# Kernel optimization log

Hardware: AMD Instinct MI355X
Metric: run time of the kernel (lower is better)

## Reference

```python
import jax, jax.numpy as jnp
import numpy as np

LN_EPS = 1e-5  # torch nn.LayerNorm default


def setup_inputs() -> dict:
    key = jax.random.key(0)
    ks = jax.random.split(key, 8)
    B, S, H, A, L = 32, 2048, 1024, 256, 10
    return {
        "hidden_states": jax.random.normal(ks[0], (B, S, H), dtype=jnp.float32),
        "language_ids": jax.random.randint(ks[1], (B,), 0, L, dtype=jnp.int64),
        "W1": jax.random.normal(ks[2], (L, H, A), dtype=jnp.float32) * (1.0 / np.sqrt(H)),
        "b1": jnp.zeros((L, A), dtype=jnp.float32),
        "W2": jax.random.normal(ks[3], (L, A, H), dtype=jnp.float32) * (1.0 / np.sqrt(A)),
        "b2": jnp.zeros((L, H), dtype=jnp.float32),
        "gamma": jnp.ones((L, H), dtype=jnp.float32),
        "beta": jnp.zeros((L, H), dtype=jnp.float32),
    }


def reference(hidden_states, language_ids, W1, b1, W2, b2, gamma, beta):
    # Gather each sample's language-specific adapter params: [B, ...]
    w1 = W1[language_ids]                       # [B, H, A]
    w2 = W2[language_ids]                       # [B, A, H]
    # Bottleneck MLP (dropout is identity at inference)
    h = jnp.einsum('bsh,bha->bsa', hidden_states, w1) + b1[language_ids][:, None, :]
    h = jax.nn.relu(h)
    adapted = jnp.einsum('bsa,bah->bsh', h, w2) + b2[language_ids][:, None, :]
    # Residual + per-language LayerNorm over last dim
    x = hidden_states + adapted
    mean = jnp.mean(x, axis=-1, keepdims=True)
    var = jnp.mean(jnp.square(x - mean), axis=-1, keepdims=True)
    normed = (x - mean) * jax.lax.rsqrt(var + LN_EPS)
    return normed * gamma[language_ids][:, None, :] + beta[language_ids][:, None, :]
```

## Files before the change

kernel.cpp:

```cpp
#include <hip/hip_runtime.h>

#define B_  32
#define S_  2048
#define H_  1024
#define A_  256
#define L_  10

typedef unsigned short u16;
typedef __bf16 bfv8 __attribute__((ext_vector_type(8)));
typedef float  f32x4 __attribute__((ext_vector_type(4)));

__device__ __forceinline__ u16 f2bf(float f) {
    unsigned int u = __builtin_bit_cast(unsigned int, f);
    u += 0x7FFFu + ((u >> 16) & 1u);
    return (u16)(u >> 16);
}
__device__ __forceinline__ float bf2f(u16 h) {
    unsigned int u = ((unsigned int)h) << 16;
    return __builtin_bit_cast(float, u);
}

__global__ __launch_bounds__(256) void pack_weights(
    const float* __restrict__ W1, const float* __restrict__ W2,
    u16* __restrict__ w1h, u16* __restrict__ w1l,
    u16* __restrict__ w2h, u16* __restrict__ w2l)
{
    int tid = blockIdx.x * 256 + threadIdx.x;
    int which = tid >= L_ * 262144;
    int p = which ? tid - L_ * 262144 : tid;
    int i = p & 7, lane = (p >> 3) & 63, lid = p >> 18;
    int kk = ((lane >> 4) << 3) + i;
    const float* src; u16 *dh, *dl;
    if (!which) {
        int ntkt = (p >> 9) & 511;
        int nt = ntkt & 15, kt = ntkt >> 4;
        int k = kt * 32 + kk, n = nt * 16 + (lane & 15);
        src = W1 + ((size_t)lid * H_ + k) * A_ + n;
        dh = w1h; dl = w1l;
    } else {
        int ntkt = (p >> 9) & 511;
        int nt = ntkt & 63, kt = ntkt >> 6;
        int k = kt * 32 + kk, n = nt * 16 + (lane & 15);
        src = W2 + ((size_t)lid * A_ + k) * H_ + n;
        dh = w2h; dl = w2l;
    }
    float w = *src;
    u16 hi = f2bf(w);
    u16 lo = f2bf(w - bf2f(hi));
    dh[p] = hi; dl[p] = lo;
}

__global__ __launch_bounds__(512) void k_gemm1(
    const float* __restrict__ X, const int* __restrict__ langs,
    const float* __restrict__ b1,
    const u16* __restrict__ w1h, const u16* __restrict__ w1l,
    u16* __restrict__ hh, u16* __restrict__ hl)
{
    __shared__ union {
        struct { u16 xh[64][72]; u16 xl[64][72]; } st;
        float hbuf[64][256];
    } lds;

    const int b   = blockIdx.y;
    const int s0  = blockIdx.x * 64;
    const int lid = langs[b];
    const int t    = threadIdx.x;
    const int lane = t & 63, wid = t >> 6;
    const int wm = wid >> 2, wn = wid & 3;
    const int lr = lane & 15, lg = lane >> 4;

    f32x4 acc[2][4];
    #pragma unroll
    for (int mf = 0; mf < 2; ++mf)
        #pragma unroll
        for (int nf = 0; nf < 4; ++nf) acc[mf][nf] = f32x4{0.f, 0.f, 0.f, 0.f};

    const float* Xb = X + ((size_t)(b * S_ + s0)) * H_;

    #pragma unroll 1
    for (int kc = 0; kc < 16; ++kc) {
        {
            int row = t >> 3, cg = (t & 7) * 8;
            const float* src = Xb + (size_t)row * H_ + kc * 64 + cg;
            float4 v0 = *(const float4*)(src);
            float4 v1 = *(const float4*)(src + 4);
            float vv[8] = {v0.x, v0.y, v0.z, v0.w, v1.x, v1.y, v1.z, v1.w};
            u16* dh = &lds.st.xh[row][cg];
            u16* dl = &lds.st.xl[row][cg];
            #pragma unroll
            for (int j = 0; j < 8; ++j) {
                u16 h = f2bf(vv[j]);
                dh[j] = h; dl[j] = f2bf(vv[j] - bf2f(h));
            }
        }
        __syncthreads();
        #pragma unroll
        for (int kl = 0; kl < 2; ++kl) {
            bfv8 ah[2], al[2];
            #pragma unroll
            for (int mf = 0; mf < 2; ++mf) {
                int row = wm * 32 + mf * 16 + lr;
                int co  = kl * 32 + lg * 8;
                ah[mf] = *(const bfv8*)&lds.st.xh[row][co];
                al[mf] = *(const bfv8*)&lds.st.xl[row][co];
            }
            int ktg = kc * 2 + kl;
            #pragma unroll
            for (int nf = 0; nf < 4; ++nf) {
                int nt = wn * 4 + nf;
                size_t tb = (((size_t)lid * 32 + ktg) * 16 + nt) * 512 + lane * 8;
                bfv8 bh = *(const bfv8*)(w1h + tb);
                bfv8 bl = *(const bfv8*)(w1l + tb);
                #pragma unroll
                for (int mf = 0; mf < 2; ++mf) {
                    acc[mf][nf] = __builtin_amdgcn_mfma_f32_16x16x32_bf16(ah[mf], bh, acc[mf][nf], 0, 0, 0);
                    acc[mf][nf] = __builtin_amdgcn_mfma_f32_16x16x32_bf16(ah[mf], bl, acc[mf][nf], 0, 0, 0);
                    acc[mf][nf] = __builtin_amdgcn_mfma_f32_16x16x32_bf16(al[mf], bh, acc[mf][nf], 0, 0, 0);
                }
            }
        }
        __syncthreads();
    }

    #pragma unroll
    for (int mf = 0; mf < 2; ++mf)
        #pragma unroll
        for (int nf = 0; nf < 4; ++nf) {
            int col = wn * 64 + nf * 16 + lr;
            float bias = b1[lid * A_ + col];
            #pragma unroll
            for (int r = 0; r < 4; ++r) {
                int row = wm * 32 + mf * 16 + lg * 4 + r;
                float v = acc[mf][nf][r] + bias;
                v = v > 0.f ? v : 0.f;
                lds.hbuf[row][col ^ ((row & 7) << 2)] = v;
            }
        }
    __syncthreads();

    size_t base = (((size_t)b * 128 + (s0 >> 4)) * 8) * 512;
    #pragma unroll
    for (int j = 0; j < 32; ++j) {
        int q  = t + j * 512;
        int i  = q & 7, lp = (q >> 3) & 63, kt = (q >> 9) & 7, mt = q >> 12;
        int rowl = mt * 16 + (lp & 15);
        int k    = kt * 32 + ((lp >> 4) << 3) + i;
        float v = lds.hbuf[rowl][k ^ ((rowl & 7) << 2)];
        u16 hi = f2bf(v);
        u16 lo = f2bf(v - bf2f(hi));
        hh[base + q] = hi;
        hl[base + q] = lo;
    }
}

__global__ __launch_bounds__(512) void k_gemm2(
    const float* __restrict__ X, const int* __restrict__ langs,
    const float* __restrict__ b2, const float* __restrict__ gamma,
    const float* __restrict__ beta,
    const u16* __restrict__ w2h, const u16* __restrict__ w2l,
    const u16* __restrict__ hh, const u16* __restrict__ hl,
    float* __restrict__ out)
{
    __shared__ float part[64][4][2];
    __shared__ float mrstd[64][2];

    const int b   = blockIdx.y;
    const int s0  = blockIdx.x * 64;
    const int lid = langs[b];
    const int t    = threadIdx.x;
    const int lane = t & 63, wid = t >> 6;
    const int wm = wid >> 2, wn = wid & 3;
    const int lr = lane & 15, lg = lane >> 4;

    f32x4 acc[2][16];
    #pragma unroll
    for (int mf = 0; mf < 2; ++mf)
        #pragma unroll
        for (int nf = 0; nf < 16; ++nf) acc[mf][nf] = f32x4{0.f, 0.f, 0.f, 0.f};

    size_t habase = (((size_t)b * 128 + (s0 >> 4) + wm * 2) * 8) * 512;

    #pragma unroll 1
    for (int kt = 0; kt < 8; ++kt) {
        bfv8 ah[2], al[2];
        #pragma unroll
        for (int mf = 0; mf < 2; ++mf) {
            size_t tb = habase + ((size_t)mf * 8 + kt) * 512 + lane * 8;
            ah[mf] = *(const bfv8*)(hh + tb);
            al[mf] = *(const bfv8*)(hl + tb);
        }
        #pragma unroll
        for (int nf = 0; nf < 16; ++nf) {
            int nt = wn * 16 + nf;
            size_t tb = (((size_t)lid * 8 + kt) * 64 + nt) * 512 + lane * 8;
            bfv8 bh = *(const bfv8*)(w2h + tb);
            bfv8 bl = *(const bfv8*)(w2l + tb);
            #pragma unroll
            for (int mf = 0; mf < 2; ++mf) {
                acc[mf][nf] = __builtin_amdgcn_mfma_f32_16x16x32_bf16(ah[mf], bh, acc[mf][nf], 0, 0, 0);
                acc[mf][nf] = __builtin_amdgcn_mfma_f32_16x16x32_bf16(ah[mf], bl, acc[mf][nf], 0, 0, 0);
                acc[mf][nf] = __builtin_amdgcn_mfma_f32_16x16x32_bf16(al[mf], bh, acc[mf][nf], 0, 0, 0);
            }
        }
    }

    const float* Xb = X + ((size_t)(b * S_ + s0)) * H_;
    float s1[2][4], s2[2][4];
    #pragma unroll
    for (int mf = 0; mf < 2; ++mf)
        #pragma unroll
        for (int r = 0; r < 4; ++r) { s1[mf][r] = 0.f; s2[mf][r] = 0.f; }

    #pragma unroll
    for (int mf = 0; mf < 2; ++mf)
        #pragma unroll
        for (int nf = 0; nf < 16; ++nf) {
            int col = wn * 256 + nf * 16 + lr;
            float bb = b2[lid * H_ + col];
            #pragma unroll
            for (int r = 0; r < 4; ++r) {
                int row = wm * 32 + mf * 16 + lg * 4 + r;
                float x = acc[mf][nf][r] + bb + Xb[(size_t)row * H_ + col];
                acc[mf][nf][r] = x;
                s1[mf][r] += x; s2[mf][r] += x * x;
            }
        }

    #pragma unroll
    for (int mf = 0; mf < 2; ++mf)
        #pragma unroll
        for (int r = 0; r < 4; ++r) {
            float a = s1[mf][r], c = s2[mf][r];
            #pragma unroll
            for (int m = 1; m < 16; m <<= 1) { a += __shfl_xor(a, m); c += __shfl_xor(c, m); }
            if (lr == 0) {
                int row = wm * 32 + mf * 16 + lg * 4 + r;
                part[row][wn][0] = a; part[row][wn][1] = c;
            }
        }
    __syncthreads();
    if (t < 64) {
        float a = part[t][0][0] + part[t][1][0] + part[t][2][0] + part[t][3][0];
        float c = part[t][0][1] + part[t][1][1] + part[t][2][1] + part[t][3][1];
        float mean = a * (1.f / 1024.f);
        float var  = c * (1.f / 1024.f) - mean * mean;
        mrstd[t][0] = mean;
        mrstd[t][1] = rsqrtf(var + 1e-5f);
    }
    __syncthreads();

    float* ob = out + ((size_t)(b * S_ + s0)) * H_;
    #pragma unroll
    for (int nf = 0; nf < 16; ++nf) {
        int col = wn * 256 + nf * 16 + lr;
        float g  = gamma[lid * H_ + col];
        float bt = beta[lid * H_ + col];
        #pragma unroll
        for (int mf = 0; mf < 2; ++mf)
            #pragma unroll
            for (int r = 0; r < 4; ++r) {
                int row = wm * 32 + mf * 16 + lg * 4 + r;
                float x = acc[mf][nf][r];
                ob[(size_t)row * H_ + col] = (x - mrstd[row][0]) * mrstd[row][1] * g + bt;
            }
    }
}

extern "C" void kernel_launch(void* const* d_in, const int* in_sizes, int n_in,
                              void* d_out, int out_size, void* d_ws, size_t ws_size,
                              hipStream_t stream)
{
    const float* X     = (const float*)d_in[0];
    const int*   langs = (const int*)  d_in[1];
    const float* W1    = (const float*)d_in[2];
    const float* b1    = (const float*)d_in[3];
    const float* W2    = (const float*)d_in[4];
    const float* b2    = (const float*)d_in[5];
    const float* gamma = (const float*)d_in[6];
    const float* beta  = (const float*)d_in[7];
    float* out = (float*)d_out;

    char* ws = (char*)d_ws;
    u16* w1h = (u16*)(ws);
    u16* w1l = (u16*)(ws + 5242880);
    u16* w2h = (u16*)(ws + 10485760);
    u16* w2l = (u16*)(ws + 15728640);
    u16* hh  = (u16*)(ws + 20971520);
    u16* hl  = (u16*)(ws + 54525952);

    hipLaunchKernelGGL(pack_weights, dim3(20480), dim3(256), 0, stream,
                       W1, W2, w1h, w1l, w2h, w2l);
    hipLaunchKernelGGL(k_gemm1, dim3(S_ / 64, B_), dim3(512), 0, stream,
                       X, langs, b1, w1h, w1l, hh, hl);
    hipLaunchKernelGGL(k_gemm2, dim3(S_ / 64, B_), dim3(512), 0, stream,
                       X, langs, b2, gamma, beta, w2h, w2l, hh, hl, out);
}
```

Before: 783.4 us.

## Fuse both adapter GEMMs into one kernel with LDS-staged, double-buffered weights

Merges the two GEMM kernels into one so the bottleneck activation stays in shared memory as split bf16 hi/lo planes instead of going through global memory. Weight tiles are staged into LDS with asynchronous global-to-LDS loads, double-buffered against the MFMA work, and the X tile for the next k-step is prefetched in registers. The packing kernel is rewritten to read weights in coalesced tiles through LDS, and blocks are remapped across batches. In exchange it uses about 148KB of dynamic LDS, which limits occupancy to one block per CU, and adds a barrier per k-step.

```diff
diff --git a/kernel.cpp b/kernel.cpp
--- a/kernel.cpp
+++ b/kernel.cpp
@@ -7,8 +7,10 @@
 #define L_  10
 
 typedef unsigned short u16;
-typedef __bf16 bfv8 __attribute__((ext_vector_type(8)));
+typedef __bf16 bf16_t;
+typedef bf16_t bfv8 __attribute__((ext_vector_type(8)));
 typedef float  f32x4 __attribute__((ext_vector_type(4)));
+typedef u16    u16x4 __attribute__((ext_vector_type(4)));
 
 __device__ __forceinline__ u16 f2bf(float f) {
     unsigned int u = __builtin_bit_cast(unsigned int, f);
@@ -18,6 +20,21 @@
 __device__ __forceinline__ float bf2f(u16 h) {
     unsigned int u = ((unsigned int)h) << 16;
     return __builtin_bit_cast(float, u);
+}
+
+typedef __attribute__((address_space(1))) const unsigned int gu32_t;
+typedef __attribute__((address_space(3))) unsigned int lu32_t;
+__device__ __forceinline__ void glds16(const void* g, void* l) {
+    __builtin_amdgcn_global_load_lds((gu32_t*)g, (lu32_t*)l, 16, 0, 0);
+}
+
+__device__ __forceinline__ void split4(float4 v, u16x4& h4, u16x4& l4) {
+    float a0 = v.x, a1 = v.y, a2 = v.z, a3 = v.w;
+    u16 h;
+    h = f2bf(a0); h4[0] = h; l4[0] = f2bf(a0 - bf2f(h));
+    h = f2bf(a1); h4[1] = h; l4[1] = f2bf(a1 - bf2f(h));
+    h = f2bf(a2); h4[2] = h; l4[2] = f2bf(a2 - bf2f(h));
+    h = f2bf(a3); h4[3] = h; l4[3] = f2bf(a3 - bf2f(h));
 }
 
 __global__ __launch_bounds__(256) void pack_weights(
@@ -25,99 +42,134 @@
     u16* __restrict__ w1h, u16* __restrict__ w1l,
     u16* __restrict__ w2h, u16* __restrict__ w2l)
 {
-    int tid = blockIdx.x * 256 + threadIdx.x;
-    int which = tid >= L_ * 262144;
-    int p = which ? tid - L_ * 262144 : tid;
-    int i = p & 7, lane = (p >> 3) & 63, lid = p >> 18;
-    int kk = ((lane >> 4) << 3) + i;
-    const float* src; u16 *dh, *dl;
-    if (!which) {
-        int ntkt = (p >> 9) & 511;
-        int nt = ntkt & 15, kt = ntkt >> 4;
-        int k = kt * 32 + kk, n = nt * 16 + (lane & 15);
-        src = W1 + ((size_t)lid * H_ + k) * A_ + n;
+    __shared__ float lds[32][264];
+    const int p = blockIdx.x;
+    const float* src; int sstride; u16 *dh, *dl; size_t dbase;
+    if (p < 320) {
+        int lid = p >> 5, ktg = p & 31;
+        src = W1 + ((size_t)lid * H_ + ktg * 32) * A_;
+        sstride = A_;
         dh = w1h; dl = w1l;
+        dbase = (size_t)(lid * 32 + ktg) * 8192;
     } else {
-        int ntkt = (p >> 9) & 511;
-        int nt = ntkt & 63, kt = ntkt >> 6;
-        int k = kt * 32 + kk, n = nt * 16 + (lane & 15);
-        src = W2 + ((size_t)lid * A_ + k) * H_ + n;
+        int p2 = p - 320;
+        int lid = p2 >> 5, kt = (p2 >> 2) & 7, nq = p2 & 3;
+        src = W2 + ((size_t)lid * A_ + kt * 32) * H_ + nq * 256;
+        sstride = H_;
         dh = w2h; dl = w2l;
-    }
-    float w = *src;
-    u16 hi = f2bf(w);
-    u16 lo = f2bf(w - bf2f(hi));
-    dh[p] = hi; dl[p] = lo;
-}
-
-__global__ __launch_bounds__(512) void k_gemm1(
+        dbase = ((size_t)(lid * 8 + kt) * 64 + nq * 16) * 512;
+    }
+    const int t = threadIdx.x;
+    #pragma unroll
+    for (int j = 0; j < 8; ++j) {
+        int row = j * 4 + (t >> 6);
+        int c4  = (t & 63) * 4;
+        float4 v = *(const float4*)(src + (size_t)row * sstride + c4);
+        *(float4*)&lds[row][c4] = v;
+    }
+    __syncthreads();
+    #pragma unroll
+    for (int j = 0; j < 32; ++j) {
+        int q    = j * 256 + t;
+        int slot = q & 511, tl = q >> 9;
+        int ln   = slot >> 3, i = slot & 7;
+        int kl   = ((ln >> 4) << 3) + i;
+        int n    = tl * 16 + (ln & 15);
+        float v  = lds[kl][n];
+        u16 hi   = f2bf(v);
+        dh[dbase + q] = hi;
+        dl[dbase + q] = f2bf(v - bf2f(hi));
+    }
+}
+
+__global__ __launch_bounds__(512) void fused_adapter(
     const float* __restrict__ X, const int* __restrict__ langs,
-    const float* __restrict__ b1,
+    const float* __restrict__ b1, const float* __restrict__ b2,
+    const float* __restrict__ gamma, const float* __restrict__ beta,
     const u16* __restrict__ w1h, const u16* __restrict__ w1l,
-    u16* __restrict__ hh, u16* __restrict__ hl)
+    const u16* __restrict__ w2h, const u16* __restrict__ w2l,
+    float* __restrict__ out)
 {
-    __shared__ union {
-        struct { u16 xh[64][72]; u16 xl[64][72]; } st;
-        float hbuf[64][256];
-    } lds;
-
-    const int b   = blockIdx.y;
-    const int s0  = blockIdx.x * 64;
+    extern __shared__ char smem[];
+    u16*   hh    = (u16*)smem;
+    u16*   hl    = (u16*)(smem + 32768);
+    u16*   xbuf  = (u16*)(smem + 65536);
+    u16*   w1b   = (u16*)(smem + 83968);
+    u16*   w2b   = (u16*)(smem + 65536);
+    float* part  = (float*)(smem + 149504);
+    float* mrstd = (float*)(smem + 151552);
+
+    const int fid = blockIdx.x;
+    const int uu  = fid >> 3;
+    const int b   = (fid & 7) * 4 + (uu >> 5);
+    const int s0  = (uu & 31) * 64;
     const int lid = langs[b];
-    const int t    = threadIdx.x;
-    const int lane = t & 63, wid = t >> 6;
+
+    const int t = threadIdx.x, lane = t & 63, wid = t >> 6;
     const int wm = wid >> 2, wn = wid & 3;
     const int lr = lane & 15, lg = lane >> 4;
 
-    f32x4 acc[2][4];
-    #pragma unroll
-    for (int mf = 0; mf < 2; ++mf)
-        #pragma unroll
-        for (int nf = 0; nf < 4; ++nf) acc[mf][nf] = f32x4{0.f, 0.f, 0.f, 0.f};
-
     const float* Xb = X + ((size_t)(b * S_ + s0)) * H_;
 
+    f32x4 acc1[2][4];
+    #pragma unroll
+    for (int mf = 0; mf < 2; ++mf)
+        #pragma unroll
+        for (int nf = 0; nf < 4; ++nf) acc1[mf][nf] = f32x4{0.f, 0.f, 0.f, 0.f};
+
+    const int srow = t >> 3, skg = (t & 7) * 4;
+
+    {
+        float4 xv = *(const float4*)(Xb + (size_t)srow * H_ + skg);
+        #pragma unroll
+        for (int j = 0; j < 4; ++j) {
+            int idx = wid * 4 + j, pl = idx >> 4, nt = idx & 15;
+            const u16* g = (pl ? w1l : w1h) + ((size_t)(lid * 32 + 0) * 16 + nt) * 512 + lane * 8;
+            glds16(g, w1b + ((0 * 2 + pl) * 16 + nt) * 512);
+        }
+        u16x4 h4, l4; split4(xv, h4, l4);
+        *(u16x4*)(xbuf + srow * 72 + skg)        = h4;
+        *(u16x4*)(xbuf + 4608 + srow * 72 + skg) = l4;
+        __syncthreads();
+    }
+
     #pragma unroll 1
-    for (int kc = 0; kc < 16; ++kc) {
-        {
-            int row = t >> 3, cg = (t & 7) * 8;
-            const float* src = Xb + (size_t)row * H_ + kc * 64 + cg;
-            float4 v0 = *(const float4*)(src);
-            float4 v1 = *(const float4*)(src + 4);
-            float vv[8] = {v0.x, v0.y, v0.z, v0.w, v1.x, v1.y, v1.z, v1.w};
-            u16* dh = &lds.st.xh[row][cg];
-            u16* dl = &lds.st.xl[row][cg];
-            #pragma unroll
-            for (int j = 0; j < 8; ++j) {
-                u16 h = f2bf(vv[j]);
-                dh[j] = h; dl[j] = f2bf(vv[j] - bf2f(h));
+    for (int kt = 0; kt < 32; ++kt) {
+        float4 xv;
+        if (kt < 31) {
+            xv = *(const float4*)(Xb + (size_t)srow * H_ + (kt + 1) * 32 + skg);
+            #pragma unroll
+            for (int j = 0; j < 4; ++j) {
+                int idx = wid * 4 + j, pl = idx >> 4, nt = idx & 15;
+                const u16* g = (pl ? w1l : w1h) + ((size_t)(lid * 32 + kt + 1) * 16 + nt) * 512 + lane * 8;
+                glds16(g, w1b + ((((kt + 1) & 1) * 2 + pl) * 16 + nt) * 512);
+            }
+        }
+        bfv8 ah[2], al[2];
+        #pragma unroll
+        for (int mf = 0; mf < 2; ++mf) {
+            int row = wm * 32 + mf * 16 + lr;
+            ah[mf] = *(const bfv8*)(xbuf + row * 72 + lg * 8);
+            al[mf] = *(const bfv8*)(xbuf + 4608 + row * 72 + lg * 8);
+        }
+        const u16* wb = w1b + (kt & 1) * 16384;
+        #pragma unroll
+        for (int nf = 0; nf < 4; ++nf) {
+            int nt = wn * 4 + nf;
+            bfv8 bh = *(const bfv8*)(wb + nt * 512 + lane * 8);
+            bfv8 bl = *(const bfv8*)(wb + 8192 + nt * 512 + lane * 8);
+            #pragma unroll
+            for (int mf = 0; mf < 2; ++mf) {
+                acc1[mf][nf] = __builtin_amdgcn_mfma_f32_16x16x32_bf16(ah[mf], bh, acc1[mf][nf], 0, 0, 0);
+                acc1[mf][nf] = __builtin_amdgcn_mfma_f32_16x16x32_bf16(ah[mf], bl, acc1[mf][nf], 0, 0, 0);
+                acc1[mf][nf] = __builtin_amdgcn_mfma_f32_16x16x32_bf16(al[mf], bh, acc1[mf][nf], 0, 0, 0);
             }
         }
         __syncthreads();
-        #pragma unroll
-        for (int kl = 0; kl < 2; ++kl) {
-            bfv8 ah[2], al[2];
-            #pragma unroll
-            for (int mf = 0; mf < 2; ++mf) {
-                int row = wm * 32 + mf * 16 + lr;
-                int co  = kl * 32 + lg * 8;
-                ah[mf] = *(const bfv8*)&lds.st.xh[row][co];
-                al[mf] = *(const bfv8*)&lds.st.xl[row][co];
-            }
-            int ktg = kc * 2 + kl;
-            #pragma unroll
-            for (int nf = 0; nf < 4; ++nf) {
-                int nt = wn * 4 + nf;
-                size_t tb = (((size_t)lid * 32 + ktg) * 16 + nt) * 512 + lane * 8;
-                bfv8 bh = *(const bfv8*)(w1h + tb);
-                bfv8 bl = *(const bfv8*)(w1l + tb);
-                #pragma unroll
-                for (int mf = 0; mf < 2; ++mf) {
-                    acc[mf][nf] = __builtin_amdgcn_mfma_f32_16x16x32_bf16(ah[mf], bh, acc[mf][nf], 0, 0, 0);
-                    acc[mf][nf] = __builtin_amdgcn_mfma_f32_16x16x32_bf16(ah[mf], bl, acc[mf][nf], 0, 0, 0);
-                    acc[mf][nf] = __builtin_amdgcn_mfma_f32_16x16x32_bf16(al[mf], bh, acc[mf][nf], 0, 0, 0);
-                }
-            }
+        if (kt < 31) {
+            u16x4 h4, l4; split4(xv, h4, l4);
+            *(u16x4*)(xbuf + srow * 72 + skg)        = h4;
+            *(u16x4*)(xbuf + 4608 + srow * 72 + skg) = l4;
         }
         __syncthreads();
     }
@@ -126,144 +178,140 @@
     for (int mf = 0; mf < 2; ++mf)
         #pragma unroll
         for (int nf = 0; nf < 4; ++nf) {
-            int col = wn * 64 + nf * 16 + lr;
-            float bias = b1[lid * A_ + col];
+            int k = wn * 64 + nf * 16 + lr;
+            float bias = b1[lid * A_ + k];
             #pragma unroll
             for (int r = 0; r < 4; ++r) {
                 int row = wm * 32 + mf * 16 + lg * 4 + r;
-                float v = acc[mf][nf][r] + bias;
+                float v = acc1[mf][nf][r] + bias;
                 v = v > 0.f ? v : 0.f;
-                lds.hbuf[row][col ^ ((row & 7) << 2)] = v;
-            }
-        }
+                int sw = (row & 7) << 3;
+                u16 hi = f2bf(v);
+                hh[row * 256 + (k ^ sw)] = hi;
+                hl[row * 256 + (k ^ sw)] = f2bf(v - bf2f(hi));
+            }
+        }
+    #pragma unroll
+    for (int j = 0; j < 4; ++j) {
+        int idx = wid * 4 + j, pl = idx >> 4, tl = idx & 15;
+        const u16* g = (pl ? w2l : w2h) + ((size_t)(lid * 8 + 0) * 64 + tl) * 512 + lane * 8;
+        glds16(g, w2b + ((0 * 2 + pl) * 16 + tl) * 512);
+    }
     __syncthreads();
 
-    size_t base = (((size_t)b * 128 + (s0 >> 4)) * 8) * 512;
-    #pragma unroll
-    for (int j = 0; j < 32; ++j) {
-        int q  = t + j * 512;
-        int i  = q & 7, lp = (q >> 3) & 63, kt = (q >> 9) & 7, mt = q >> 12;
-        int rowl = mt * 16 + (lp & 15);
-        int k    = kt * 32 + ((lp >> 4) << 3) + i;
-        float v = lds.hbuf[rowl][k ^ ((rowl & 7) << 2)];
-        u16 hi = f2bf(v);
-        u16 lo = f2bf(v - bf2f(hi));
-        hh[base + q] = hi;
-        hl[base + q] = lo;
-    }
-}
-
-__global__ __launch_bounds__(512) void k_gemm2(
-    const float* __restrict__ X, const int* __restrict__ langs,
-    const float* __restrict__ b2, const float* __restrict__ gamma,
-    const float* __restrict__ beta,
-    const u16* __restrict__ w2h, const u16* __restrict__ w2l,
-    const u16* __restrict__ hh, const u16* __restrict__ hl,
-    float* __restrict__ out)
-{
-    __shared__ float part[64][4][2];
-    __shared__ float mrstd[64][2];
-
-    const int b   = blockIdx.y;
-    const int s0  = blockIdx.x * 64;
-    const int lid = langs[b];
-    const int t    = threadIdx.x;
-    const int lane = t & 63, wid = t >> 6;
-    const int wm = wid >> 2, wn = wid & 3;
-    const int lr = lane & 15, lg = lane >> 4;
-
-    f32x4 acc[2][16];
-    #pragma unroll
-    for (int mf = 0; mf < 2; ++mf)
-        #pragma unroll
-        for (int nf = 0; nf < 16; ++nf) acc[mf][nf] = f32x4{0.f, 0.f, 0.f, 0.f};
-
-    size_t habase = (((size_t)b * 128 + (s0 >> 4) + wm * 2) * 8) * 512;
-
-    #pragma unroll 1
+    f32x4 acc2[2][4][4];
+    #pragma unroll
+    for (int mf = 0; mf < 2; ++mf)
+        #pragma unroll
+        for (int q = 0; q < 4; ++q)
+            #pragma unroll
+            for (int nf = 0; nf < 4; ++nf) acc2[mf][q][nf] = f32x4{0.f, 0.f, 0.f, 0.f};
+
+    bfv8 a2h[2], a2l[2];
+    #pragma unroll
     for (int kt = 0; kt < 8; ++kt) {
-        bfv8 ah[2], al[2];
-        #pragma unroll
-        for (int mf = 0; mf < 2; ++mf) {
-            size_t tb = habase + ((size_t)mf * 8 + kt) * 512 + lane * 8;
-            ah[mf] = *(const bfv8*)(hh + tb);
-            al[mf] = *(const bfv8*)(hl + tb);
-        }
-        #pragma unroll
-        for (int nf = 0; nf < 16; ++nf) {
-            int nt = wn * 16 + nf;
-            size_t tb = (((size_t)lid * 8 + kt) * 64 + nt) * 512 + lane * 8;
-            bfv8 bh = *(const bfv8*)(w2h + tb);
-            bfv8 bl = *(const bfv8*)(w2l + tb);
-            #pragma unroll
-            for (int mf = 0; mf < 2; ++mf) {
-                acc[mf][nf] = __builtin_amdgcn_mfma_f32_16x16x32_bf16(ah[mf], bh, acc[mf][nf], 0, 0, 0);
-                acc[mf][nf] = __builtin_amdgcn_mfma_f32_16x16x32_bf16(ah[mf], bl, acc[mf][nf], 0, 0, 0);
-                acc[mf][nf] = __builtin_amdgcn_mfma_f32_16x16x32_bf16(al[mf], bh, acc[mf][nf], 0, 0, 0);
-            }
-        }
-    }
-
-    const float* Xb = X + ((size_t)(b * S_ + s0)) * H_;
-    float s1[2][4], s2[2][4];
-    #pragma unroll
-    for (int mf = 0; mf < 2; ++mf)
-        #pragma unroll
-        for (int r = 0; r < 4; ++r) { s1[mf][r] = 0.f; s2[mf][r] = 0.f; }
-
-    #pragma unroll
-    for (int mf = 0; mf < 2; ++mf)
-        #pragma unroll
-        for (int nf = 0; nf < 16; ++nf) {
-            int col = wn * 256 + nf * 16 + lr;
-            float bb = b2[lid * H_ + col];
-            #pragma unroll
-            for (int r = 0; r < 4; ++r) {
-                int row = wm * 32 + mf * 16 + lg * 4 + r;
-                float x = acc[mf][nf][r] + bb + Xb[(size_t)row * H_ + col];
-                acc[mf][nf][r] = x;
-                s1[mf][r] += x; s2[mf][r] += x * x;
-            }
-        }
+        #pragma unroll
+        for (int q = 0; q < 4; ++q) {
+            const int ph = kt * 4 + q, pbuf = ph & 1;
+            if (ph < 31) {
+                int kn = (ph + 1) >> 2, qn = (ph + 1) & 3;
+                #pragma unroll
+                for (int j = 0; j < 4; ++j) {
+                    int idx = wid * 4 + j, pl = idx >> 4, tl = idx & 15;
+                    const u16* g = (pl ? w2l : w2h) + ((size_t)(lid * 8 + kn) * 64 + qn * 16 + tl) * 512 + lane * 8;
+                    glds16(g, w2b + (((pbuf ^ 1) * 2 + pl) * 16 + tl) * 512);
+                }
+            }
+            if (q == 0) {
+                #pragma unroll
+                for (int mf = 0; mf < 2; ++mf) {
+                    int row = wm * 32 + mf * 16 + lr;
+                    int sw  = (row & 7) << 3;
+                    a2h[mf] = *(const bfv8*)(hh + row * 256 + ((kt * 32 + lg * 8) ^ sw));
+                    a2l[mf] = *(const bfv8*)(hl + row * 256 + ((kt * 32 + lg * 8) ^ sw));
+                }
+            }
+            const u16* wb2 = w2b + pbuf * 16384;
+            #pragma unroll
+            for (int nf = 0; nf < 4; ++nf) {
+                int tl = wn * 4 + nf;
+                bfv8 bh = *(const bfv8*)(wb2 + tl * 512 + lane * 8);
+                bfv8 bl = *(const bfv8*)(wb2 + 8192 + tl * 512 + lane * 8);
+                #pragma unroll
+                for (int mf = 0; mf < 2; ++mf) {
+                    acc2[mf][q][nf] = __builtin_amdgcn_mfma_f32_16x16x32_bf16(a2h[mf], bh, acc2[mf][q][nf], 0, 0, 0);
+                    acc2[mf][q][nf] = __builtin_amdgcn_mfma_f32_16x16x32_bf16(a2h[mf], bl, acc2[mf][q][nf], 0, 0, 0);
+                    acc2[mf][q][nf] = __builtin_amdgcn_mfma_f32_16x16x32_bf16(a2l[mf], bh, acc2[mf][q][nf], 0, 0, 0);
+                }
+            }
+            __syncthreads();
+        }
+    }
+
+    float s1v[2][4], s2v[2][4];
+    #pragma unroll
+    for (int mf = 0; mf < 2; ++mf)
+        #pragma unroll
+        for (int r = 0; r < 4; ++r) { s1v[mf][r] = 0.f; s2v[mf][r] = 0.f; }
+
+    #pragma unroll
+    for (int mf = 0; mf < 2; ++mf)
+        #pragma unroll
+        for (int q = 0; q < 4; ++q)
+            #pragma unroll
+            for (int nf = 0; nf < 4; ++nf) {
+                int col = (q * 16 + wn * 4 + nf) * 16 + lr;
+                float bb = b2[lid * H_ + col];
+                #pragma unroll
+                for (int r = 0; r < 4; ++r) {
+                    int row = wm * 32 + mf * 16 + lg * 4 + r;
+                    float x = acc2[mf][q][nf][r] + bb + Xb[(size_t)row * H_ + col];
+                    acc2[mf][q][nf][r] = x;
+                    s1v[mf][r] += x; s2v[mf][r] += x * x;
+                }
+            }
 
     #pragma unroll
     for (int mf = 0; mf < 2; ++mf)
         #pragma unroll
         for (int r = 0; r < 4; ++r) {
-            float a = s1[mf][r], c = s2[mf][r];
+            float a = s1v[mf][r], c = s2v[mf][r];
             #pragma unroll
             for (int m = 1; m < 16; m <<= 1) { a += __shfl_xor(a, m); c += __shfl_xor(c, m); }
             if (lr == 0) {
                 int row = wm * 32 + mf * 16 + lg * 4 + r;
-                part[row][wn][0] = a; part[row][wn][1] = c;
+                part[(row * 4 + wn) * 2 + 0] = a;
+                part[(row * 4 + wn) * 2 + 1] = c;
             }
         }
     __syncthreads();
     if (t < 64) {
-        float a = part[t][0][0] + part[t][1][0] + part[t][2][0] + part[t][3][0];
-        float c = part[t][0][1] + part[t][1][1] + part[t][2][1] + part[t][3][1];
+        float a = part[(t*4+0)*2] + part[(t*4+1)*2] + part[(t*4+2)*2] + part[(t*4+3)*2];
+        float c = part[(t*4+0)*2+1] + part[(t*4+1)*2+1] + part[(t*4+2)*2+1] + part[(t*4+3)*2+1];
         float mean = a * (1.f / 1024.f);
         float var  = c * (1.f / 1024.f) - mean * mean;
-        mrstd[t][0] = mean;
-        mrstd[t][1] = rsqrtf(var + 1e-5f);
+        mrstd[t*2]   = mean;
+        mrstd[t*2+1] = rsqrtf(var + 1e-5f);
     }
     __syncthreads();
 
     float* ob = out + ((size_t)(b * S_ + s0)) * H_;
     #pragma unroll
-    for (int nf = 0; nf < 16; ++nf) {
-        int col = wn * 256 + nf * 16 + lr;
-        float g  = gamma[lid * H_ + col];
-        float bt = beta[lid * H_ + col];
-        #pragma unroll
-        for (int mf = 0; mf < 2; ++mf)
-            #pragma unroll
-            for (int r = 0; r < 4; ++r) {
-                int row = wm * 32 + mf * 16 + lg * 4 + r;
-                float x = acc[mf][nf][r];
-                ob[(size_t)row * H_ + col] = (x - mrstd[row][0]) * mrstd[row][1] * g + bt;
-            }
-    }
+    for (int q = 0; q < 4; ++q)
+        #pragma unroll
+        for (int nf = 0; nf < 4; ++nf) {
+            int col = (q * 16 + wn * 4 + nf) * 16 + lr;
+            float g  = gamma[lid * H_ + col];
+            float bt = beta[lid * H_ + col];
+            #pragma unroll
+            for (int mf = 0; mf < 2; ++mf)
+                #pragma unroll
+                for (int r = 0; r < 4; ++r) {
+                    int row = wm * 32 + mf * 16 + lg * 4 + r;
+                    float x = acc2[mf][q][nf][r];
+                    ob[(size_t)row * H_ + col] = (x - mrstd[row*2]) * mrstd[row*2+1] * g + bt;
+                }
+        }
 }
 
 extern "C" void kernel_launch(void* const* d_in, const int* in_sizes, int n_in,
@@ -285,13 +333,12 @@
     u16* w1l = (u16*)(ws + 5242880);
     u16* w2h = (u16*)(ws + 10485760);
     u16* w2l = (u16*)(ws + 15728640);
-    u16* hh  = (u16*)(ws + 20971520);
-    u16* hl  = (u16*)(ws + 54525952);
-
-    hipLaunchKernelGGL(pack_weights, dim3(20480), dim3(256), 0, stream,
+
+    hipFuncSetAttribute((const void*)fused_adapter,
+                        hipFuncAttributeMaxDynamicSharedMemorySize, 152064);
+
+    hipLaunchKernelGGL(pack_weights, dim3(640), dim3(256), 0, stream,
                        W1, W2, w1h, w1l, w2h, w2l);
-    hipLaunchKernelGGL(k_gemm1, dim3(S_ / 64, B_), dim3(512), 0, stream,
-                       X, langs, b1, w1h, w1l, hh, hl);
-    hipLaunchKernelGGL(k_gemm2, dim3(S_ / 64, B_), dim3(512), 0, stream,
-                       X, langs, b2, gamma, beta, w2h, w2l, hh, hl, out);
-}
+    hipLaunchKernelGGL(fused_adapter, dim3(1024), dim3(512), 152064, stream,
+                       X, langs, b1, b2, gamma, beta, w1h, w1l, w2h, w2l, out);
+}
```

Result: slower. 885.7 us (+13.1%).
